# Optimization experiments

Hardware: AMD Instinct MI355X
Metric: run time of the kernel (lower is better)

The kernel has to match this reference:

```python
import jax, jax.numpy as jnp
import numpy as np

N, C, H, W = 8, 256, 64, 64
Q_REDUCE, K_REDUCE, V_REDUCE = 8, 8, 1


def setup_inputs() -> dict:
    key = jax.random.key(0)
    ks = jax.random.split(key, 6)
    Cq, Ck, Cv = C // Q_REDUCE, C // K_REDUCE, C // V_REDUCE
    s = 0.02
    x = jax.random.normal(ks[0], (N, C, H, W), dtype=jnp.float32)
    Wq = jax.random.normal(ks[1], (Cq, C), dtype=jnp.float32) * s
    Wk = jax.random.normal(ks[2], (Ck, C), dtype=jnp.float32) * s
    Wv = jax.random.normal(ks[3], (Cv, C), dtype=jnp.float32) * s
    Wo = jax.random.normal(ks[4], (C, Cv), dtype=jnp.float32) * s
    gamma = jax.random.normal(ks[5], (), dtype=jnp.float32)  # trained scalar (init 0.0 in torch)
    return {"x": x, "Wq": Wq, "Wk": Wk, "Wv": Wv, "Wo": Wo, "gamma": gamma}


def reference(x, Wq, Wk, Wv, Wo, gamma):
    n, c, h, w = x.shape
    xf = x.reshape(n, c, h * w)                      # [N, C, HW]
    q = jnp.einsum('qc,ncl->nql', Wq, xf)            # [N, Cq, HW] (1x1 conv)
    k = jnp.einsum('kc,ncl->nkl', Wk, xf)            # [N, Ck, HW]
    v = jnp.einsum('vc,ncl->nvl', Wv, xf)            # [N, Cv, HW]
    e = jnp.einsum('nci,ncj->nij', q, k)             # [N, HW, HW], unscaled energies
    a = jax.nn.softmax(e, axis=-1)                   # softmax over keys j
    o = jnp.einsum('nvi,nij->nvj', v, a)             # [N, Cv, HW]  (o = bmm(v, a))
    o = o.reshape(n, -1, w, h)                       # faithful: view(N,-1,W,H)
    out = jnp.einsum('ov,nvhw->nohw', Wo, o)         # output 1x1 conv
    return gamma * out
```

## Files before the change

kernel.cpp:

```cpp
#include <hip/hip_runtime.h>
#include <hip/hip_bf16.h>

#define NB 8
#define CIN 256
#define LL 4096
#define CQ 32
#define CV 256

typedef __attribute__((ext_vector_type(8))) short bf16x8;
typedef __attribute__((ext_vector_type(4))) float f32x4;

__device__ __forceinline__ unsigned short f2bf(float f) {
    union { __hip_bfloat16 h; unsigned short u; } c;
    c.h = __float2bfloat16(f);
    return c.u;
}
__device__ __forceinline__ unsigned int f2bf2(float a, float b) {
    union { __hip_bfloat162 h; unsigned int u; } c;
    float2 f; f.x = a; f.y = b;
    c.h = __float22bfloat162_rn(f);
    return c.u;
}
__device__ __forceinline__ float bf2f(unsigned short h) {
    return __uint_as_float(((unsigned)h) << 16);
}

__global__ __launch_bounds__(256) void k_wcast(
    const float* __restrict__ Wq, const float* __restrict__ Wk,
    const float* __restrict__ Wv, const float* __restrict__ Wo,
    unsigned short* __restrict__ Wb, unsigned short* __restrict__ Wob)
{
    const int row = blockIdx.x, t = threadIdx.x;
    if (row < 320) {
        const float* src = row < 32 ? Wq + row * 256
                         : row < 64 ? Wk + (row - 32) * 256
                                    : Wv + (row - 64) * 256;
        Wb[row * 256 + t] = f2bf(src[t]);
    } else {
        const int r2 = row - 320;
        Wob[r2 * 256 + t] = f2bf(Wo[r2 * 256 + t]);
    }
}

__global__ __launch_bounds__(256) void k_qkv2(
    const float* __restrict__ x, const unsigned short* __restrict__ Wb,
    unsigned short* __restrict__ qkt, unsigned short* __restrict__ v)
{
    __shared__ unsigned short xlds[64][264];
    const int n = blockIdx.y, l0 = blockIdx.x * 64, t = threadIdx.x;
    const int w = t >> 6, lane = t & 63, lid = lane & 15, quad = lane >> 4;

    #pragma unroll
    for (int part = 0; part < 8; part++) {
        const int cbase = part * 32 + w * 8;
        float tmp[8];
        #pragma unroll
        for (int cc = 0; cc < 8; cc++)
            tmp[cc] = x[(n * CIN + cbase + cc) * LL + l0 + lane];
        bf16x8 s;
        #pragma unroll
        for (int cc = 0; cc < 8; cc++) s[cc] = (short)f2bf(tmp[cc]);
        *(bf16x8*)&xlds[lane][cbase] = s;
    }
    __syncthreads();

    const f32x4 fzero = {0.f, 0.f, 0.f, 0.f};
    f32x4 acc[5][4];
    #pragma unroll
    for (int mt = 0; mt < 5; mt++)
        #pragma unroll
        for (int nt = 0; nt < 4; nt++) acc[mt][nt] = fzero;

    for (int k0 = 0; k0 < 256; k0 += 32) {
        bf16x8 bx[4];
        #pragma unroll
        for (int nt = 0; nt < 4; nt++)
            bx[nt] = *(const bf16x8*)&xlds[nt * 16 + lid][k0 + quad * 8];
        #pragma unroll
        for (int mt = 0; mt < 5; mt++) {
            const bf16x8 wa = *(const bf16x8*)&Wb[(w * 80 + mt * 16 + lid) * 256 + k0 + quad * 8];
            #pragma unroll
            for (int nt = 0; nt < 4; nt++)
                acc[mt][nt] = __builtin_amdgcn_mfma_f32_16x16x32_bf16(wa, bx[nt], acc[mt][nt], 0, 0, 0);
        }
    }
    #pragma unroll
    for (int mt = 0; mt < 5; mt++)
        #pragma unroll
        for (int nt = 0; nt < 4; nt++)
            #pragma unroll
            for (int reg = 0; reg < 4; reg++) {
                const int r = w * 80 + mt * 16 + quad * 4 + reg;
                const int l = l0 + nt * 16 + lid;
                const unsigned short val = f2bf(acc[mt][nt][reg]);
                if (r < 64) qkt[(n * LL + l) * 64 + r] = val;
                else        v[(n * CV + (r - 64)) * LL + l] = val;
            }
}

__global__ __launch_bounds__(256) void k_rowsum2(
    const unsigned short* __restrict__ qkt, float* __restrict__ rl)
{
    __shared__ float red[64];
    const int n = blockIdx.y, i0 = blockIdx.x * 64, t = threadIdx.x;
    const int w = t >> 6, lane = t & 63, lid = lane & 15, quad = lane >> 4;
    if (t < 64) red[t] = 0.f;
    __syncthreads();

    bf16x8 aq[4];
    #pragma unroll
    for (int mt = 0; mt < 4; mt++)
        aq[mt] = *(const bf16x8*)&qkt[(n * LL + i0 + mt * 16 + lid) * 64 + quad * 8];

    const f32x4 fzero = {0.f, 0.f, 0.f, 0.f};
    float sums[4][4];
    #pragma unroll
    for (int mt = 0; mt < 4; mt++)
        #pragma unroll
        for (int reg = 0; reg < 4; reg++) sums[mt][reg] = 0.f;

    for (int jt = 0; jt < 16; jt++) {
        const int j0 = jt * 256 + w * 64;
        bf16x8 bk[4];
        #pragma unroll
        for (int nt = 0; nt < 4; nt++)
            bk[nt] = *(const bf16x8*)&qkt[(n * LL + j0 + nt * 16 + lid) * 64 + 32 + quad * 8];
        #pragma unroll
        for (int mt = 0; mt < 4; mt++)
            #pragma unroll
            for (int nt = 0; nt < 4; nt++) {
                f32x4 e = __builtin_amdgcn_mfma_f32_16x16x32_bf16(aq[mt], bk[nt], fzero, 0, 0, 0);
                sums[mt][0] += __expf(e[0]);
                sums[mt][1] += __expf(e[1]);
                sums[mt][2] += __expf(e[2]);
                sums[mt][3] += __expf(e[3]);
            }
    }
    #pragma unroll
    for (int mt = 0; mt < 4; mt++)
        #pragma unroll
        for (int reg = 0; reg < 4; reg++) {
            float s = sums[mt][reg];
            s += __shfl_xor(s, 1); s += __shfl_xor(s, 2);
            s += __shfl_xor(s, 4); s += __shfl_xor(s, 8);
            if (lid == 0) atomicAdd(&red[mt * 16 + quad * 4 + reg], s);
        }
    __syncthreads();
    if (t < 64) rl[n * LL + i0 + t] = 1.0f / red[t];
}

__global__ __launch_bounds__(256) void k_attn2(
    const unsigned short* __restrict__ qkt, const unsigned short* __restrict__ v,
    const float* __restrict__ rl, unsigned short* __restrict__ o)
{
    __shared__ unsigned short plds[64][64];
    const int n = blockIdx.z, vh = blockIdx.y, j0 = blockIdx.x * 64, t = threadIdx.x;
    const int w = t >> 6, lane = t & 63, lid = lane & 15, quad = lane >> 4;
    const int xkey = lid & 7;

    bf16x8 bk[4];
    #pragma unroll
    for (int nt = 0; nt < 4; nt++)
        bk[nt] = *(const bf16x8*)&qkt[(n * LL + j0 + nt * 16 + lid) * 64 + 32 + quad * 8];

    const f32x4 fzero = {0.f, 0.f, 0.f, 0.f};
    f32x4 acc[2][4];
    #pragma unroll
    for (int mt = 0; mt < 2; mt++)
        #pragma unroll
        for (int nt = 0; nt < 4; nt++) acc[mt][nt] = fzero;

    for (int ic = 0; ic < 64; ic++) {
        const int i0 = ic * 64;
        const bf16x8 aq = *(const bf16x8*)&qkt[(n * LL + i0 + w * 16 + lid) * 64 + quad * 8];
        const float4 rl4 = *(const float4*)&rl[n * LL + i0 + w * 16 + quad * 4];
        __syncthreads();
        #pragma unroll
        for (int nt = 0; nt < 4; nt++) {
            f32x4 e = __builtin_amdgcn_mfma_f32_16x16x32_bf16(aq, bk[nt], fzero, 0, 0, 0);
            const unsigned a01 = f2bf2(__expf(e[0]) * rl4.x, __expf(e[1]) * rl4.y);
            const unsigned a23 = f2bf2(__expf(e[2]) * rl4.z, __expf(e[3]) * rl4.w);
            const int chunk = (2 * w + (quad >> 1)) ^ xkey;
            unsigned* p = (unsigned*)&plds[nt * 16 + lid][chunk * 8 + (quad & 1) * 4];
            p[0] = a01; p[1] = a23;
        }
        __syncthreads();
        #pragma unroll
        for (int h = 0; h < 2; h++) {
            bf16x8 bp[4];
            #pragma unroll
            for (int nt = 0; nt < 4; nt++) {
                const int chunk = (4 * h + quad) ^ xkey;
                bp[nt] = *(const bf16x8*)&plds[nt * 16 + lid][chunk * 8];
            }
            #pragma unroll
            for (int mt = 0; mt < 2; mt++) {
                const bf16x8 av = *(const bf16x8*)
                    &v[(n * CV + vh * 128 + w * 32 + mt * 16 + lid) * LL + i0 + h * 32 + quad * 8];
                #pragma unroll
                for (int nt = 0; nt < 4; nt++)
                    acc[mt][nt] = __builtin_amdgcn_mfma_f32_16x16x32_bf16(av, bp[nt], acc[mt][nt], 0, 0, 0);
            }
        }
    }
    #pragma unroll
    for (int mt = 0; mt < 2; mt++)
        #pragma unroll
        for (int nt = 0; nt < 4; nt++)
            #pragma unroll
            for (int reg = 0; reg < 4; reg++)
                o[(n * CV + vh * 128 + w * 32 + mt * 16 + quad * 4 + reg) * LL + j0 + nt * 16 + lid] =
                    f2bf(acc[mt][nt][reg]);
}

__global__ __launch_bounds__(256) void k_out2(
    const unsigned short* __restrict__ o, const unsigned short* __restrict__ Wob,
    const float* __restrict__ gp, float* __restrict__ out)
{
    __shared__ unsigned short olds[64][264];
    const int n = blockIdx.y, l0 = blockIdx.x * 64, t = threadIdx.x;
    const int w = t >> 6, lane = t & 63, lid = lane & 15, quad = lane >> 4;

    #pragma unroll
    for (int part = 0; part < 8; part++) {
        const int cbase = part * 32 + w * 8;
        bf16x8 s;
        #pragma unroll
        for (int cc = 0; cc < 8; cc++)
            s[cc] = (short)o[(n * CV + cbase + cc) * LL + l0 + lane];
        *(bf16x8*)&olds[lane][cbase] = s;
    }
    __syncthreads();

    const f32x4 fzero = {0.f, 0.f, 0.f, 0.f};
    f32x4 acc[4][4];
    #pragma unroll
    for (int mt = 0; mt < 4; mt++)
        #pragma unroll
        for (int nt = 0; nt < 4; nt++) acc[mt][nt] = fzero;

    for (int k0 = 0; k0 < 256; k0 += 32) {
        bf16x8 bo[4];
        #pragma unroll
        for (int nt = 0; nt < 4; nt++)
            bo[nt] = *(const bf16x8*)&olds[nt * 16 + lid][k0 + quad * 8];
        #pragma unroll
        for (int mt = 0; mt < 4; mt++) {
            const bf16x8 wa = *(const bf16x8*)&Wob[(w * 64 + mt * 16 + lid) * 256 + k0 + quad * 8];
            #pragma unroll
            for (int nt = 0; nt < 4; nt++)
                acc[mt][nt] = __builtin_amdgcn_mfma_f32_16x16x32_bf16(wa, bo[nt], acc[mt][nt], 0, 0, 0);
        }
    }
    const float g = *gp;
    #pragma unroll
    for (int mt = 0; mt < 4; mt++)
        #pragma unroll
        for (int nt = 0; nt < 4; nt++)
            #pragma unroll
            for (int reg = 0; reg < 4; reg++) {
                const int r = w * 64 + mt * 16 + quad * 4 + reg;
                out[(n * CIN + r) * LL + l0 + nt * 16 + lid] = g * acc[mt][nt][reg];
            }
}

extern "C" void kernel_launch(void* const* d_in, const int* in_sizes, int n_in,
                              void* d_out, int out_size, void* d_ws, size_t ws_size,
                              hipStream_t stream) {
    const float* x     = (const float*)d_in[0];
    const float* Wq    = (const float*)d_in[1];
    const float* Wk    = (const float*)d_in[2];
    const float* Wv    = (const float*)d_in[3];
    const float* Wo    = (const float*)d_in[4];
    const float* gamma = (const float*)d_in[5];

    unsigned short* qkt = (unsigned short*)d_ws;
    unsigned short* v   = qkt + (size_t)NB * LL * 64;
    unsigned short* o   = v + (size_t)NB * CV * LL;
    unsigned short* Wb  = o + (size_t)NB * CV * LL;
    unsigned short* Wob = Wb + 320 * 256;
    float* rl           = (float*)(Wob + 256 * 256);
    float* out = (float*)d_out;

    k_wcast  <<<dim3(576),      256, 0, stream>>>(Wq, Wk, Wv, Wo, Wb, Wob);
    k_qkv2   <<<dim3(64, 8),    256, 0, stream>>>(x, Wb, qkt, v);
    k_rowsum2<<<dim3(64, 8),    256, 0, stream>>>(qkt, rl);
    k_attn2  <<<dim3(64, 2, 8), 256, 0, stream>>>(qkt, v, rl, o);
    k_out2   <<<dim3(64, 8),    256, 0, stream>>>(o, Wob, gamma, out);
}
```

Before: 306.5 us.

## Pipeline attention kernel with double-buffered P tile and exp2-folded normalization

New measurement: 297.9 us. 2.8% less time.

```diff
diff --git a/kernel.cpp b/kernel.cpp
--- a/kernel.cpp
+++ b/kernel.cpp
@@ -21,21 +21,20 @@
     c.h = __float22bfloat162_rn(f);
     return c.u;
 }
-__device__ __forceinline__ float bf2f(unsigned short h) {
-    return __uint_as_float(((unsigned)h) << 16);
-}
 
 __global__ __launch_bounds__(256) void k_wcast(
     const float* __restrict__ Wq, const float* __restrict__ Wk,
     const float* __restrict__ Wv, const float* __restrict__ Wo,
     unsigned short* __restrict__ Wb, unsigned short* __restrict__ Wob)
 {
+    const float LOG2E = 1.4426950408889634f;
     const int row = blockIdx.x, t = threadIdx.x;
     if (row < 320) {
-        const float* src = row < 32 ? Wq + row * 256
-                         : row < 64 ? Wk + (row - 32) * 256
-                                    : Wv + (row - 64) * 256;
-        Wb[row * 256 + t] = f2bf(src[t]);
+        float val;
+        if (row < 32)      val = Wq[row * 256 + t] * LOG2E;
+        else if (row < 64) val = Wk[(row - 32) * 256 + t];
+        else               val = Wv[(row - 64) * 256 + t];
+        Wb[row * 256 + t] = f2bf(val);
     } else {
         const int r2 = row - 320;
         Wob[r2 * 256 + t] = f2bf(Wo[r2 * 256 + t]);
@@ -47,6 +46,7 @@
     unsigned short* __restrict__ qkt, unsigned short* __restrict__ v)
 {
     __shared__ unsigned short xlds[64][264];
+    __shared__ unsigned short tr[64][72];
     const int n = blockIdx.y, l0 = blockIdx.x * 64, t = threadIdx.x;
     const int w = t >> 6, lane = t & 63, lid = lane & 15, quad = lane >> 4;
 
@@ -78,28 +78,39 @@
             bx[nt] = *(const bf16x8*)&xlds[nt * 16 + lid][k0 + quad * 8];
         #pragma unroll
         for (int mt = 0; mt < 5; mt++) {
-            const bf16x8 wa = *(const bf16x8*)&Wb[(w * 80 + mt * 16 + lid) * 256 + k0 + quad * 8];
+            const int row = (mt == 0) ? (w * 16 + lid) : (64 + w * 64 + (mt - 1) * 16 + lid);
+            const bf16x8 wa = *(const bf16x8*)&Wb[row * 256 + k0 + quad * 8];
             #pragma unroll
             for (int nt = 0; nt < 4; nt++)
                 acc[mt][nt] = __builtin_amdgcn_mfma_f32_16x16x32_bf16(wa, bx[nt], acc[mt][nt], 0, 0, 0);
         }
     }
     #pragma unroll
-    for (int mt = 0; mt < 5; mt++)
+    for (int mt = 1; mt < 5; mt++)
         #pragma unroll
         for (int nt = 0; nt < 4; nt++)
             #pragma unroll
             for (int reg = 0; reg < 4; reg++) {
-                const int r = w * 80 + mt * 16 + quad * 4 + reg;
-                const int l = l0 + nt * 16 + lid;
-                const unsigned short val = f2bf(acc[mt][nt][reg]);
-                if (r < 64) qkt[(n * LL + l) * 64 + r] = val;
-                else        v[(n * CV + (r - 64)) * LL + l] = val;
+                const int vr = w * 64 + (mt - 1) * 16 + quad * 4 + reg;
+                v[((size_t)n * CV + vr) * LL + l0 + nt * 16 + lid] = f2bf(acc[mt][nt][reg]);
             }
+    #pragma unroll
+    for (int nt = 0; nt < 4; nt++)
+        #pragma unroll
+        for (int reg = 0; reg < 4; reg++)
+            tr[nt * 16 + lid][w * 16 + quad * 4 + reg] = f2bf(acc[0][nt][reg]);
+    __syncthreads();
+    {
+        const int l = t >> 2, c = (t & 3) * 16;
+        uint4 d0 = *(const uint4*)&tr[l][c];
+        uint4 d1 = *(const uint4*)&tr[l][c + 8];
+        uint4* dst = (uint4*)&qkt[((size_t)n * LL + l0 + l) * 64 + c];
+        dst[0] = d0; dst[1] = d1;
+    }
 }
 
 __global__ __launch_bounds__(256) void k_rowsum2(
-    const unsigned short* __restrict__ qkt, float* __restrict__ rl)
+    const unsigned short* __restrict__ qkt, float* __restrict__ lns)
 {
     __shared__ float red[64];
     const int n = blockIdx.y, i0 = blockIdx.x * 64, t = threadIdx.x;
@@ -110,7 +121,7 @@
     bf16x8 aq[4];
     #pragma unroll
     for (int mt = 0; mt < 4; mt++)
-        aq[mt] = *(const bf16x8*)&qkt[(n * LL + i0 + mt * 16 + lid) * 64 + quad * 8];
+        aq[mt] = *(const bf16x8*)&qkt[((size_t)n * LL + i0 + mt * 16 + lid) * 64 + quad * 8];
 
     const f32x4 fzero = {0.f, 0.f, 0.f, 0.f};
     float sums[4][4];
@@ -124,16 +135,16 @@
         bf16x8 bk[4];
         #pragma unroll
         for (int nt = 0; nt < 4; nt++)
-            bk[nt] = *(const bf16x8*)&qkt[(n * LL + j0 + nt * 16 + lid) * 64 + 32 + quad * 8];
+            bk[nt] = *(const bf16x8*)&qkt[((size_t)n * LL + j0 + nt * 16 + lid) * 64 + 32 + quad * 8];
         #pragma unroll
         for (int mt = 0; mt < 4; mt++)
             #pragma unroll
             for (int nt = 0; nt < 4; nt++) {
                 f32x4 e = __builtin_amdgcn_mfma_f32_16x16x32_bf16(aq[mt], bk[nt], fzero, 0, 0, 0);
-                sums[mt][0] += __expf(e[0]);
-                sums[mt][1] += __expf(e[1]);
-                sums[mt][2] += __expf(e[2]);
-                sums[mt][3] += __expf(e[3]);
+                sums[mt][0] += __builtin_exp2f(e[0]);
+                sums[mt][1] += __builtin_exp2f(e[1]);
+                sums[mt][2] += __builtin_exp2f(e[2]);
+                sums[mt][3] += __builtin_exp2f(e[3]);
             }
     }
     #pragma unroll
@@ -146,70 +157,115 @@
             if (lid == 0) atomicAdd(&red[mt * 16 + quad * 4 + reg], s);
         }
     __syncthreads();
-    if (t < 64) rl[n * LL + i0 + t] = 1.0f / red[t];
-}
-
-__global__ __launch_bounds__(256) void k_attn2(
+    if (t < 64) lns[n * LL + i0 + t] = -__builtin_log2f(red[t]);
+}
+
+__device__ __forceinline__ void write_p(unsigned short (*pl)[64], const f32x4* e,
+                                        int w, int lid, int quad, int xkey)
+{
+    #pragma unroll
+    for (int nt = 0; nt < 4; nt++) {
+        const unsigned a01 = f2bf2(__builtin_exp2f(e[nt][0]), __builtin_exp2f(e[nt][1]));
+        const unsigned a23 = f2bf2(__builtin_exp2f(e[nt][2]), __builtin_exp2f(e[nt][3]));
+        const int chunk = (2 * w + (quad >> 1)) ^ xkey;
+        unsigned* p = (unsigned*)&pl[nt * 16 + lid][chunk * 8 + (quad & 1) * 4];
+        p[0] = a01; p[1] = a23;
+    }
+}
+
+__global__ __launch_bounds__(256) void k_attn3(
     const unsigned short* __restrict__ qkt, const unsigned short* __restrict__ v,
-    const float* __restrict__ rl, unsigned short* __restrict__ o)
-{
-    __shared__ unsigned short plds[64][64];
-    const int n = blockIdx.z, vh = blockIdx.y, j0 = blockIdx.x * 64, t = threadIdx.x;
+    const float* __restrict__ lns, unsigned short* __restrict__ o)
+{
+    __shared__ unsigned short plds[2][64][64];
+    const int n = blockIdx.y, j0 = blockIdx.x * 64, t = threadIdx.x;
     const int w = t >> 6, lane = t & 63, lid = lane & 15, quad = lane >> 4;
     const int xkey = lid & 7;
 
+    const unsigned short* qrow = qkt + ((size_t)n * LL + w * 16 + lid) * 64 + quad * 8;
+    const float* lrow = lns + (size_t)n * LL + w * 16 + quad * 4;
+    const unsigned short* vrow = v + ((size_t)n * CV + w * 64 + lid) * LL + quad * 8;
+
     bf16x8 bk[4];
     #pragma unroll
     for (int nt = 0; nt < 4; nt++)
-        bk[nt] = *(const bf16x8*)&qkt[(n * LL + j0 + nt * 16 + lid) * 64 + 32 + quad * 8];
+        bk[nt] = *(const bf16x8*)&qkt[((size_t)n * LL + j0 + nt * 16 + lid) * 64 + 32 + quad * 8];
 
     const f32x4 fzero = {0.f, 0.f, 0.f, 0.f};
-    f32x4 acc[2][4];
-    #pragma unroll
-    for (int mt = 0; mt < 2; mt++)
+    f32x4 acc[4][4];
+    #pragma unroll
+    for (int mt = 0; mt < 4; mt++)
         #pragma unroll
         for (int nt = 0; nt < 4; nt++) acc[mt][nt] = fzero;
 
-    for (int ic = 0; ic < 64; ic++) {
-        const int i0 = ic * 64;
-        const bf16x8 aq = *(const bf16x8*)&qkt[(n * LL + i0 + w * 16 + lid) * 64 + quad * 8];
-        const float4 rl4 = *(const float4*)&rl[n * LL + i0 + w * 16 + quad * 4];
-        __syncthreads();
-        #pragma unroll
-        for (int nt = 0; nt < 4; nt++) {
-            f32x4 e = __builtin_amdgcn_mfma_f32_16x16x32_bf16(aq, bk[nt], fzero, 0, 0, 0);
-            const unsigned a01 = f2bf2(__expf(e[0]) * rl4.x, __expf(e[1]) * rl4.y);
-            const unsigned a23 = f2bf2(__expf(e[2]) * rl4.z, __expf(e[3]) * rl4.w);
-            const int chunk = (2 * w + (quad >> 1)) ^ xkey;
-            unsigned* p = (unsigned*)&plds[nt * 16 + lid][chunk * 8 + (quad & 1) * 4];
-            p[0] = a01; p[1] = a23;
-        }
-        __syncthreads();
+    bf16x8 aq = *(const bf16x8*)qrow;
+    f32x4 lnsC = *(const f32x4*)lrow;
+    {
+        f32x4 e[4];
+        #pragma unroll
+        for (int nt = 0; nt < 4; nt++)
+            e[nt] = __builtin_amdgcn_mfma_f32_16x16x32_bf16(aq, bk[nt], lnsC, 0, 0, 0);
+        aq = *(const bf16x8*)(qrow + (size_t)64 * 64);
+        lnsC = *(const f32x4*)(lrow + 64);
+        write_p(plds[0], e, w, lid, quad, xkey);
+    }
+    bf16x8 av[8];
+    #pragma unroll
+    for (int h = 0; h < 2; h++)
+        #pragma unroll
+        for (int mt = 0; mt < 4; mt++)
+            av[h * 4 + mt] = *(const bf16x8*)(vrow + (size_t)mt * 16 * LL + h * 32);
+    __syncthreads();
+
+    for (int ic = 0; ic < 63; ic++) {
+        const int cur = ic & 1;
+        const size_t i0 = (size_t)ic * 64;
+        f32x4 e2[4];
+        #pragma unroll
+        for (int nt = 0; nt < 4; nt++)
+            e2[nt] = __builtin_amdgcn_mfma_f32_16x16x32_bf16(aq, bk[nt], lnsC, 0, 0, 0);
+        const size_t ipf = (ic < 62) ? (i0 + 128) : i0;
+        aq = *(const bf16x8*)(qrow + ipf * 64);
+        lnsC = *(const f32x4*)(lrow + ipf);
         #pragma unroll
         for (int h = 0; h < 2; h++) {
             bf16x8 bp[4];
             #pragma unroll
-            for (int nt = 0; nt < 4; nt++) {
-                const int chunk = (4 * h + quad) ^ xkey;
-                bp[nt] = *(const bf16x8*)&plds[nt * 16 + lid][chunk * 8];
-            }
-            #pragma unroll
-            for (int mt = 0; mt < 2; mt++) {
-                const bf16x8 av = *(const bf16x8*)
-                    &v[(n * CV + vh * 128 + w * 32 + mt * 16 + lid) * LL + i0 + h * 32 + quad * 8];
+            for (int nt = 0; nt < 4; nt++)
+                bp[nt] = *(const bf16x8*)&plds[cur][nt * 16 + lid][((4 * h + quad) ^ xkey) * 8];
+            #pragma unroll
+            for (int mt = 0; mt < 4; mt++)
                 #pragma unroll
                 for (int nt = 0; nt < 4; nt++)
-                    acc[mt][nt] = __builtin_amdgcn_mfma_f32_16x16x32_bf16(av, bp[nt], acc[mt][nt], 0, 0, 0);
-            }
+                    acc[mt][nt] = __builtin_amdgcn_mfma_f32_16x16x32_bf16(av[h * 4 + mt], bp[nt], acc[mt][nt], 0, 0, 0);
         }
-    }
-    #pragma unroll
-    for (int mt = 0; mt < 2; mt++)
+        #pragma unroll
+        for (int h = 0; h < 2; h++)
+            #pragma unroll
+            for (int mt = 0; mt < 4; mt++)
+                av[h * 4 + mt] = *(const bf16x8*)(vrow + (size_t)mt * 16 * LL + (i0 + 64) + h * 32);
+        write_p(plds[cur ^ 1], e2, w, lid, quad, xkey);
+        __syncthreads();
+    }
+    #pragma unroll
+    for (int h = 0; h < 2; h++) {
+        bf16x8 bp[4];
+        #pragma unroll
+        for (int nt = 0; nt < 4; nt++)
+            bp[nt] = *(const bf16x8*)&plds[1][nt * 16 + lid][((4 * h + quad) ^ xkey) * 8];
+        #pragma unroll
+        for (int mt = 0; mt < 4; mt++)
+            #pragma unroll
+            for (int nt = 0; nt < 4; nt++)
+                acc[mt][nt] = __builtin_amdgcn_mfma_f32_16x16x32_bf16(av[h * 4 + mt], bp[nt], acc[mt][nt], 0, 0, 0);
+    }
+    #pragma unroll
+    for (int mt = 0; mt < 4; mt++)
         #pragma unroll
         for (int nt = 0; nt < 4; nt++)
             #pragma unroll
             for (int reg = 0; reg < 4; reg++)
-                o[(n * CV + vh * 128 + w * 32 + mt * 16 + quad * 4 + reg) * LL + j0 + nt * 16 + lid] =
+                o[((size_t)n * CV + w * 64 + mt * 16 + quad * 4 + reg) * LL + j0 + nt * 16 + lid] =
                     f2bf(acc[mt][nt][reg]);
 }
 
@@ -227,7 +283,7 @@
         bf16x8 s;
         #pragma unroll
         for (int cc = 0; cc < 8; cc++)
-            s[cc] = (short)o[(n * CV + cbase + cc) * LL + l0 + lane];
+            s[cc] = (short)o[((size_t)n * CV + cbase + cc) * LL + l0 + lane];
         *(bf16x8*)&olds[lane][cbase] = s;
     }
     __syncthreads();
@@ -260,7 +316,7 @@
             #pragma unroll
             for (int reg = 0; reg < 4; reg++) {
                 const int r = w * 64 + mt * 16 + quad * 4 + reg;
-                out[(n * CIN + r) * LL + l0 + nt * 16 + lid] = g * acc[mt][nt][reg];
+                out[((size_t)n * CIN + r) * LL + l0 + nt * 16 + lid] = g * acc[mt][nt][reg];
             }
 }
 
@@ -279,12 +335,12 @@
     unsigned short* o   = v + (size_t)NB * CV * LL;
     unsigned short* Wb  = o + (size_t)NB * CV * LL;
     unsigned short* Wob = Wb + 320 * 256;
-    float* rl           = (float*)(Wob + 256 * 256);
+    float* lns          = (float*)(Wob + 256 * 256);
     float* out = (float*)d_out;
 
-    k_wcast  <<<dim3(576),      256, 0, stream>>>(Wq, Wk, Wv, Wo, Wb, Wob);
-    k_qkv2   <<<dim3(64, 8),    256, 0, stream>>>(x, Wb, qkt, v);
-    k_rowsum2<<<dim3(64, 8),    256, 0, stream>>>(qkt, rl);
-    k_attn2  <<<dim3(64, 2, 8), 256, 0, stream>>>(qkt, v, rl, o);
-    k_out2   <<<dim3(64, 8),    256, 0, stream>>>(o, Wob, gamma, out);
-}
+    k_wcast  <<<dim3(576),   256, 0, stream>>>(Wq, Wk, Wv, Wo, Wb, Wob);
+    k_qkv2   <<<dim3(64, 8), 256, 0, stream>>>(x, Wb, qkt, v);
+    k_rowsum2<<<dim3(64, 8), 256, 0, stream>>>(qkt, lns);
+    k_attn3  <<<dim3(64, 8), 256, 0, stream>>>(qkt, v, lns, o);
+    k_out2   <<<dim3(64, 8), 256, 0, stream>>>(o, Wob, gamma, out);
+}
```
